# Kernel optimization log

Hardware: AMD Instinct MI355X
Metric: run time of the kernel (lower is better)

Reference implementation:

```python
import jax, jax.numpy as jnp
import numpy as np
from jax import lax

HIDDEN = 1024; HEADS = 16; HEAD = 64; LAYERS = 4; MLP = 4096
PATCH = 16; TUBE = 2; CROP = 224; FRAMES = 16
GRID = CROP // PATCH          # 14
DEPTH = FRAMES // TUBE        # 8
N_TOK = DEPTH * GRID * GRID   # 1568
EPS = 1e-6
D_ROT = 2 * ((HEAD // 3) // 2)  # 20 per rotary axis (d, h, w); 4 dims left unrotated


def setup_inputs() -> dict:
    key = jax.random.key(0)
    ks = jax.random.split(key, 12)
    w = lambda k, shape: jax.random.normal(k, shape, jnp.float32) * 0.02
    L, H, M = LAYERS, HIDDEN, MLP
    return {
        "pixel_values_videos": jax.random.normal(ks[0], (2, FRAMES, 3, CROP, CROP), jnp.float32),
        "patch_w": w(ks[1], (H, 3, TUBE, PATCH, PATCH)),  # Conv3d OIDHW
        "patch_b": jnp.zeros((H,), jnp.float32),
        "ln1_g": jnp.ones((L, H), jnp.float32), "ln1_b": jnp.zeros((L, H), jnp.float32),
        "qw": w(ks[2], (L, H, H)), "qb": jnp.zeros((L, H), jnp.float32),
        "kw": w(ks[3], (L, H, H)), "kb": jnp.zeros((L, H), jnp.float32),
        "vw": w(ks[4], (L, H, H)), "vb": jnp.zeros((L, H), jnp.float32),
        "pw": w(ks[5], (L, H, H)), "pb": jnp.zeros((L, H), jnp.float32),
        "ln2_g": jnp.ones((L, H), jnp.float32), "ln2_b": jnp.zeros((L, H), jnp.float32),
        "fc1w": w(ks[6], (L, M, H)), "fc1b": jnp.zeros((L, M), jnp.float32),
        "fc2w": w(ks[7], (L, H, M)), "fc2b": jnp.zeros((L, H), jnp.float32),
        "lnf_g": jnp.ones((H,), jnp.float32), "lnf_b": jnp.zeros((H,), jnp.float32),
    }


def _layer_norm(x, g, b):
    mu = jnp.mean(x, axis=-1, keepdims=True)
    var = jnp.mean(jnp.square(x - mu), axis=-1, keepdims=True)
    return (x - mu) * lax.rsqrt(var + EPS) * g + b


def _position_ids():
    ids = jnp.arange(N_TOK)
    tpf = GRID * GRID
    d_pos = ids // tpf
    rem = ids - d_pos * tpf
    h_pos = rem // GRID
    w_pos = rem - h_pos * GRID
    return d_pos, h_pos, w_pos


def _rotate(x, pos):
    # x: (B, H, N, D); matches VJEPA2 rotate_queries_or_keys:
    # tiled (not interleaved) sin/cos * interleaved rotate-half.
    D = x.shape[-1]
    omega = 1.0 / (10000.0 ** (jnp.arange(D // 2, dtype=x.dtype) / (D / 2.0)))
    freq = pos.astype(x.dtype)[:, None] * omega              # (N, D/2)
    sin = jnp.concatenate([jnp.sin(freq)] * 2, axis=-1)      # (N, D) tiled (torch .repeat)
    cos = jnp.concatenate([jnp.cos(freq)] * 2, axis=-1)
    y = x.reshape(x.shape[:-1] + (D // 2, 2))
    y = jnp.stack([-y[..., 1], y[..., 0]], axis=-1).reshape(x.shape)
    return x * cos + y * sin


def _apply_rope(x, pos_ids):
    d_pos, h_pos, w_pos = pos_ids
    s0, s1, s2 = 0, D_ROT, 2 * D_ROT
    parts = [_rotate(x[..., s0:s1], d_pos), _rotate(x[..., s1:s2], h_pos),
             _rotate(x[..., s2:3 * D_ROT], w_pos)]
    if 3 * D_ROT < HEAD:
        parts.append(x[..., 3 * D_ROT:])
    return jnp.concatenate(parts, axis=-1)


def _forward(pixel_values_videos, patch_w, patch_b, ln1_g, ln1_b, qw, qb, kw, kb,
             vw, vb, pw, pb, ln2_g, ln2_b, fc1w, fc1b, fc2w, fc2b, lnf_g, lnf_b):
    B = pixel_values_videos.shape[0]
    x = jnp.transpose(pixel_values_videos, (0, 2, 1, 3, 4))  # (B, C, T, H, W)
    h = lax.conv_general_dilated(x, patch_w, window_strides=(TUBE, PATCH, PATCH),
                                 padding="VALID",
                                 dimension_numbers=("NCDHW", "OIDHW", "NCDHW"))
    h = h + patch_b[None, :, None, None, None]
    h = h.reshape(B, HIDDEN, -1).transpose(0, 2, 1)          # (B, N, HIDDEN)

    pos_ids = _position_ids()
    scale = HEAD ** -0.5

    for i in range(LAYERS):
        # attention block
        xn = _layer_norm(h, ln1_g[i], ln1_b[i])
        def heads(w_, b_):
            return (xn @ w_.T + b_).reshape(B, N_TOK, HEADS, HEAD).transpose(0, 2, 1, 3)
        q = _apply_rope(heads(qw[i], qb[i]), pos_ids)
        k = _apply_rope(heads(kw[i], kb[i]), pos_ids)
        v = heads(vw[i], vb[i])
        aw = jnp.einsum("bhnd,bhmd->bhnm", q, k) * scale
        aw = jax.nn.softmax(aw.astype(jnp.float32), axis=-1).astype(q.dtype)
        o = jnp.einsum("bhnm,bhmd->bhnd", aw, v)
        o = o.transpose(0, 2, 1, 3).reshape(B, N_TOK, HIDDEN)
        h = h + (o @ pw[i].T + pb[i])
        # MLP block
        xn = _layer_norm(h, ln2_g[i], ln2_b[i])
        m = jax.nn.gelu(xn @ fc1w[i].T + fc1b[i], approximate=False)
        h = h + (m @ fc2w[i].T + fc2b[i])

    return _layer_norm(h, lnf_g, lnf_b)


def reference(pixel_values_videos, patch_w, patch_b, ln1_g, ln1_b, qw, qb, kw, kb,
              vw, vb, pw, pb, ln2_g, ln2_b, fc1w, fc1b, fc2w, fc2b, lnf_g, lnf_b):
    return _forward(pixel_values_videos, patch_w, patch_b, ln1_g, ln1_b, qw, qb, kw, kb,
                    vw, vb, pw, pb, ln2_g, ln2_b, fc1w, fc1b, fc2w, fc2b, lnf_g, lnf_b)
```

## Files before the change

### kernel.cpp

```cpp
#include <hip/hip_runtime.h>
#include <math.h>

#define NTOK   1568
#define BATCH  2
#define HID    1024
#define MLPD   4096
#define NLAYER 4
#define ROWS   (BATCH*NTOK)
#define CONVK  1536

typedef __bf16 bf16x8 __attribute__((ext_vector_type(8)));
typedef __bf16 bf16x2 __attribute__((ext_vector_type(2)));
typedef float  f32x4  __attribute__((ext_vector_type(4)));

__device__ __forceinline__ unsigned short f2b(float f) {
  unsigned int u = __float_as_uint(f);
  unsigned int r = u + 0x7FFFu + ((u >> 16) & 1u);
  return (unsigned short)(r >> 16);
}
__device__ __forceinline__ float b2f(unsigned short s) {
  return __uint_as_float((unsigned int)s << 16);
}
__device__ __forceinline__ unsigned cvt2(float a, float b) {
  bf16x2 t;
  t[0] = (__bf16)a;
  t[1] = (__bf16)b;
  return __builtin_bit_cast(unsigned, t);
}
__device__ __forceinline__ float e2(float x) { return __builtin_amdgcn_exp2f(x); }

__device__ __forceinline__ void async16(const unsigned short* g, unsigned short* l) {
  __builtin_amdgcn_global_load_lds(
      (__attribute__((address_space(1))) void*)(void*)g,
      (__attribute__((address_space(3))) void*)(void*)l, 16, 0, 0);
}

__global__ __launch_bounds__(256) void cast4_k(const float* __restrict__ s,
                                               unsigned short* __restrict__ d,
                                               long long n4) {
  long long i = (long long)blockIdx.x * 256 + threadIdx.x;
  long long stride = (long long)gridDim.x * 256;
  for (; i < n4; i += stride) {
    float4 v = ((const float4*)s)[i];
    *(ushort4*)(d + i * 4) = make_ushort4(f2b(v.x), f2b(v.y), f2b(v.z), f2b(v.w));
  }
}

__global__ __launch_bounds__(256) void castqkv_k(const float* __restrict__ q,
                                                 const float* __restrict__ k,
                                                 const float* __restrict__ v,
                                                 unsigned short* __restrict__ dst) {
  const float* src = blockIdx.y == 0 ? q : (blockIdx.y == 1 ? k : v);
  long long i4 = (long long)blockIdx.x * 256 + threadIdx.x;
  long long e = i4 * 4;
  int layer = (int)(e >> 20);
  long long de = e + ((long long)(2 * layer + blockIdx.y) << 20);
  float4 val = ((const float4*)src)[i4];
  *(ushort4*)(dst + de) = make_ushort4(f2b(val.x), f2b(val.y), f2b(val.z), f2b(val.w));
}

__global__ __launch_bounds__(256) void biascat_k(const float* __restrict__ qb,
                                                 const float* __restrict__ kb,
                                                 const float* __restrict__ vb,
                                                 float* __restrict__ dst) {
  int idx = blockIdx.x * 256 + threadIdx.x;
  int layer = idx / 3072, c = idx % 3072;
  float v = c < 1024 ? qb[layer * 1024 + c]
            : (c < 2048 ? kb[layer * 1024 + c - 1024] : vb[layer * 1024 + c - 2048]);
  dst[idx] = v;
}

__global__ __launch_bounds__(256) void im2col_k(const float* __restrict__ pv,
                                                unsigned short* __restrict__ A) {
  int idx = blockIdx.x * 256 + threadIdx.x;
  int row = idx / CONVK, col = idx % CONVK;
  int b = row / NTOK, t = row % NTOK;
  int d = t / 196, r = t % 196, hh = r / 14, ww = r % 14;
  int c = col >> 9, r2 = col & 511, td = r2 >> 8, ph = (r2 >> 4) & 15, pw = r2 & 15;
  int frame = 2 * d + td;
  const float* src = pv + ((((long long)b * 16 + frame) * 3 + c) * 224 + (hh * 16 + ph)) * 224
                        + (ww * 16 + pw);
  A[idx] = f2b(*src);
}

__global__ __launch_bounds__(512, 2) void gemm256(const unsigned short* __restrict__ A,
                                                  const unsigned short* __restrict__ B,
                                                  unsigned short* outP,
                                                  int M, int N, int K, int kChunk,
                                                  size_t zStride) {
  __shared__ unsigned short As[3][256 * 32];
  __shared__ unsigned short Bs[3][256 * 32];
  const int tid = threadIdx.x;
  const int lane = tid & 63;
  const int w = tid >> 6;
  const int wr = w >> 2, wc = w & 3;
  const int l15 = lane & 15, l4 = lane >> 4;
  const int wbase = tid & ~63;

  const int gx = gridDim.x, gy = gridDim.y;
  const int nwg = gx * gy * (int)gridDim.z;
  int orig = blockIdx.x + gx * (blockIdx.y + gy * blockIdx.z);
  int q = nwg >> 3, r = nwg & 7, xcd = orig & 7, idx = orig >> 3;
  int swz = (xcd < r ? xcd * (q + 1) : r * (q + 1) + (xcd - r) * q) + idx;
  const int bn = swz % gx;
  int tmp = swz / gx;
  const int bm = tmp % gy;
  const int bz = tmp / gy;
  const int kbeg = bz * kChunk;

  const int r0 = tid >> 2;
  const int g0 = (tid & 3) ^ ((tid >> 3) & 3);
  const int i1 = 512 + tid;
  const int r1 = i1 >> 2;
  const int g1 = (tid & 3) ^ ((i1 >> 3) & 3);
  int ra0 = bm * 256 + r0; if (ra0 >= M) ra0 = M - 1;
  int ra1 = bm * 256 + r1; if (ra1 >= M) ra1 = M - 1;
  const int rb0 = bn * 256 + r0;
  const int rb1 = bn * 256 + r1;
  const size_t Ao0 = (size_t)ra0 * K + g0 * 8;
  const size_t Ao1 = (size_t)ra1 * K + g1 * 8;
  const size_t Bo0 = (size_t)rb0 * K + g0 * 8;
  const size_t Bo1 = (size_t)rb1 * K + g1 * 8;

  auto stA = [&](int buf, int k0) {
    async16(A + Ao0 + k0, &As[buf][wbase * 8]);
    async16(A + Ao1 + k0, &As[buf][4096 + wbase * 8]);
  };
  auto stB = [&](int buf, int k0) {
    async16(B + Bo0 + k0, &Bs[buf][wbase * 8]);
    async16(B + Bo1 + k0, &Bs[buf][4096 + wbase * 8]);
  };

  f32x4 acc[8][4] = {};
  const int nk = kChunk >> 5;

  stA(0, kbeg); stB(0, kbeg);
  stA(1, kbeg + 32); stB(1, kbeg + 32);

  const int pchunk = (l4 ^ ((l15 >> 1) & 3)) * 8;
  const int abase = (wr * 128 + l15) * 32 + pchunk;
  const int bbase = (wc * 64 + l15) * 32 + pchunk;

  int cur = 0;
  for (int kt = 0; kt < nk; ++kt) {
    if (kt + 1 < nk) {
      asm volatile("s_waitcnt vmcnt(4)" ::: "memory");
    } else {
      asm volatile("s_waitcnt vmcnt(0)" ::: "memory");
    }
    __builtin_amdgcn_s_barrier();
    __builtin_amdgcn_sched_barrier(0);
    const int prebuf = cur >= 1 ? cur - 1 : 2;
    const bool doPre = (kt + 2 < nk);
    const int kpre = kbeg + (kt + 2) * 32;

    if (doPre) stA(prebuf, kpre);
    bf16x8 bfr[4], af[4];
#pragma unroll
    for (int n = 0; n < 4; ++n)
      bfr[n] = *(const bf16x8*)&Bs[cur][bbase + n * 512];
#pragma unroll
    for (int m = 0; m < 4; ++m)
      af[m] = *(const bf16x8*)&As[cur][abase + m * 512];
    __builtin_amdgcn_s_setprio(1);
#pragma unroll
    for (int m = 0; m < 4; ++m)
#pragma unroll
      for (int n = 0; n < 4; ++n)
        acc[m][n] = __builtin_amdgcn_mfma_f32_16x16x32_bf16(af[m], bfr[n], acc[m][n], 0, 0, 0);
    __builtin_amdgcn_s_setprio(0);
    __builtin_amdgcn_sched_barrier(0);

    if (doPre) stB(prebuf, kpre);
#pragma unroll
    for (int m = 0; m < 4; ++m)
      af[m] = *(const bf16x8*)&As[cur][abase + (m + 4) * 512];
    __builtin_amdgcn_s_setprio(1);
#pragma unroll
    for (int m = 0; m < 4; ++m)
#pragma unroll
      for (int n = 0; n < 4; ++n)
        acc[m + 4][n] = __builtin_amdgcn_mfma_f32_16x16x32_bf16(af[m], bfr[n], acc[m + 4][n], 0, 0, 0);
    __builtin_amdgcn_s_setprio(0);
    __builtin_amdgcn_sched_barrier(0);

    cur = cur == 2 ? 0 : cur + 1;
  }

  unsigned short* pout = outP + (size_t)bz * zStride;
#pragma unroll
  for (int m = 0; m < 8; ++m) {
    int rowb = bm * 256 + wr * 128 + m * 16 + l4 * 4;
#pragma unroll
    for (int rr2 = 0; rr2 < 4; ++rr2) {
      int rr = rowb + rr2;
      if (rr >= M) continue;
#pragma unroll
      for (int n = 0; n < 4; ++n) {
        int col = bn * 256 + wc * 64 + n * 16 + l15;
        pout[(size_t)rr * N + col] = f2b(acc[m][n][rr2]);
      }
    }
  }
}

template <int NP, int GELU>
__global__ __launch_bounds__(256) void reduceN_k(const unsigned short* p,
                                                 const float* __restrict__ bias,
                                                 unsigned short* outB,
                                                 int MN, int N, size_t pStride) {
  int i8 = blockIdx.x * 256 + threadIdx.x;
  int e = i8 * 8;
  float acc[8];
#pragma unroll
  for (int j = 0; j < 8; ++j) acc[j] = 0.0f;
#pragma unroll
  for (int pp = 0; pp < NP; ++pp) {
    const unsigned short* src = p + (size_t)pp * pStride + e;
    ushort4 a0 = *(const ushort4*)src;
    ushort4 a1 = *(const ushort4*)(src + 4);
    acc[0] += b2f(a0.x); acc[1] += b2f(a0.y); acc[2] += b2f(a0.z); acc[3] += b2f(a0.w);
    acc[4] += b2f(a1.x); acc[5] += b2f(a1.y); acc[6] += b2f(a1.z); acc[7] += b2f(a1.w);
  }
  int col = e % N;
  float4 b0 = *(const float4*)(bias + col);
  float4 b1 = *(const float4*)(bias + col + 4);
  acc[0] += b0.x; acc[1] += b0.y; acc[2] += b0.z; acc[3] += b0.w;
  acc[4] += b1.x; acc[5] += b1.y; acc[6] += b1.z; acc[7] += b1.w;
  if (GELU) {
#pragma unroll
    for (int j = 0; j < 8; ++j)
      acc[j] = 0.5f * acc[j] * (1.0f + erff(acc[j] * 0.70710678118654752f));
  }
  *(ushort4*)(outB + e) = make_ushort4(f2b(acc[0]), f2b(acc[1]), f2b(acc[2]), f2b(acc[3]));
  *(ushort4*)(outB + e + 4) = make_ushort4(f2b(acc[4]), f2b(acc[5]), f2b(acc[6]), f2b(acc[7]));
}

template <int NP, int RESID, int FINAL>
__global__ __launch_bounds__(256) void redln_k(const unsigned short* __restrict__ p,
                                               const float* __restrict__ bias,
                                               const float* resid,
                                               const float* __restrict__ g,
                                               const float* __restrict__ b,
                                               float* hOut,
                                               unsigned short* __restrict__ xnOut,
                                               float* __restrict__ fOut,
                                               size_t pStride) {
  __shared__ float red[8];
  const int row = blockIdx.x, tid = threadIdx.x;
  const int col = tid * 4;
  const size_t off = (size_t)row * HID + col;
  float v0 = 0, v1 = 0, v2 = 0, v3 = 0;
#pragma unroll
  for (int pp = 0; pp < NP; ++pp) {
    ushort4 a = *(const ushort4*)(p + (size_t)pp * pStride + off);
    v0 += b2f(a.x); v1 += b2f(a.y); v2 += b2f(a.z); v3 += b2f(a.w);
  }
  float4 bs = *(const float4*)(bias + col);
  v0 += bs.x; v1 += bs.y; v2 += bs.z; v3 += bs.w;
  if (RESID) {
    float4 r = *(const float4*)(resid + off);
    v0 += r.x; v1 += r.y; v2 += r.z; v3 += r.w;
  }
  if (!FINAL) *(float4*)(hOut + off) = make_float4(v0, v1, v2, v3);
  float s = v0 + v1 + v2 + v3;
  float q = v0 * v0 + v1 * v1 + v2 * v2 + v3 * v3;
  for (int o2 = 32; o2; o2 >>= 1) { s += __shfl_xor(s, o2); q += __shfl_xor(q, o2); }
  if ((tid & 63) == 0) { red[tid >> 6] = s; red[4 + (tid >> 6)] = q; }
  __syncthreads();
  float ts = red[0] + red[1] + red[2] + red[3];
  float tq = red[4] + red[5] + red[6] + red[7];
  float mu = ts * (1.0f / HID);
  float var = tq * (1.0f / HID) - mu * mu;
  float rs = rsqrtf(var + 1e-6f);
  float o0 = (v0 - mu) * rs * g[col + 0] + b[col + 0];
  float o1 = (v1 - mu) * rs * g[col + 1] + b[col + 1];
  float o2 = (v2 - mu) * rs * g[col + 2] + b[col + 2];
  float o3 = (v3 - mu) * rs * g[col + 3] + b[col + 3];
  if (FINAL) {
    *(float4*)(fOut + off) = make_float4(o0, o1, o2, o3);
  } else {
    *(ushort4*)(xnOut + off) = make_ushort4(f2b(o0), f2b(o1), f2b(o2), f2b(o3));
  }
}

__global__ __launch_bounds__(256) void qkvprep_k(const unsigned short* __restrict__ qkvb,
                                                 unsigned short* __restrict__ Qh,
                                                 unsigned short* __restrict__ Kh,
                                                 unsigned short* __restrict__ VT) {
  __shared__ unsigned short Vs[64 * 72];
  const int tile = blockIdx.x, bh = blockIdx.y;
  const int b = bh >> 4, head = bh & 15;
  const int tid = threadIdx.x;
  const int tl = tid >> 2, dc = tid & 3;
  const int tg = tile * 64 + tl;
  const int trc = tg < NTOK ? tg : NTOK - 1;
  const bool valid = tg < NTOK;
  const size_t srow = ((size_t)(b * NTOK + trc)) * 3072 + head * 64 + dc * 16;

  {
    uint4 v0 = *(const uint4*)(qkvb + srow + 2048);
    uint4 v1 = *(const uint4*)(qkvb + srow + 2048 + 8);
    *(uint4*)&Vs[tl * 72 + dc * 16] = v0;
    *(uint4*)&Vs[tl * 72 + dc * 16 + 8] = v1;
  }

  const int t = trc;
  const int dpos = t / 196, rem = t - dpos * 196, hpos = rem / 14, wpos = rem - hpos * 14;
  const float LG = 0.9210340371976184f;
  union V16 { uint4 u[2]; unsigned short s[16]; };
  V16 qin, kin, qout, kout;
  qin.u[0] = *(const uint4*)(qkvb + srow);
  qin.u[1] = *(const uint4*)(qkvb + srow + 8);
  kin.u[0] = *(const uint4*)(qkvb + srow + 1024);
  kin.u[1] = *(const uint4*)(qkvb + srow + 1024 + 8);
#pragma unroll
  for (int p = 0; p < 8; ++p) {
    int d0 = dc * 16 + 2 * p;
    float qx0 = b2f(qin.s[2 * p]), qx1 = b2f(qin.s[2 * p + 1]);
    float kx0 = b2f(kin.s[2 * p]), kx1 = b2f(kin.s[2 * p + 1]);
    float qo0, qo1, ko0, ko1;
    if (d0 >= 60) { qo0 = qx0; qo1 = qx1; ko0 = kx0; ko1 = kx1; }
    else {
      int region = d0 / 20;
      int j0 = d0 - region * 20;
      int pos = region == 0 ? dpos : (region == 1 ? hpos : wpos);
      float fp = (float)pos;
      int i0 = j0 % 10, i1 = (j0 + 1) % 10;
      float f0 = expf(-LG * (float)i0) * fp;
      float f1 = expf(-LG * (float)i1) * fp;
      float c0 = cosf(f0), s0 = sinf(f0), c1 = cosf(f1), s1 = sinf(f1);
      qo0 = qx0 * c0 - qx1 * s0; qo1 = qx1 * c1 + qx0 * s1;
      ko0 = kx0 * c0 - kx1 * s0; ko1 = kx1 * c1 + kx0 * s1;
    }
    const float QS = 0.18033688011112042f;
    qout.s[2 * p]     = f2b(qo0 * QS);
    qout.s[2 * p + 1] = f2b(qo1 * QS);
    kout.s[2 * p]     = f2b(ko0);
    kout.s[2 * p + 1] = f2b(ko1);
  }
  if (valid) {
    size_t drow = ((size_t)bh * NTOK + tg) * 64 + dc * 16;
    *(uint4*)(Qh + drow)     = qout.u[0];
    *(uint4*)(Qh + drow + 8) = qout.u[1];
    *(uint4*)(Kh + drow)     = kout.u[0];
    *(uint4*)(Kh + drow + 8) = kout.u[1];
  }
  __syncthreads();
  {
    int d = tid >> 2, tc = tid & 3;
    if (tile * 64 + tc * 16 < NTOK) {
      V16 o;
#pragma unroll
      for (int jj = 0; jj < 16; ++jj) o.s[jj] = Vs[(tc * 16 + jj) * 72 + d];
      unsigned short* dst = VT + ((size_t)bh * 64 + d) * NTOK + tile * 64 + tc * 16;
      *(uint4*)dst = o.u[0];
      *(uint4*)(dst + 8) = o.u[1];
    }
  }
}

__global__ __launch_bounds__(256, 4) void flash5_k(const unsigned short* __restrict__ Qh,
                                                   const unsigned short* __restrict__ Kh,
                                                   const unsigned short* __restrict__ VT,
                                                   unsigned short* __restrict__ Opart,
                                                   float2* __restrict__ ml) {
  __shared__ unsigned short Ks[2][64 * 64];
  __shared__ unsigned short Vs[2][64 * 64];
  const int bh = blockIdx.x, qt = blockIdx.y, kv = blockIdx.z;
  const int kt0 = kv ? 13 : 0, kt1 = kv ? 25 : 13;
  const int tid = threadIdx.x, lane = tid & 63, w = tid >> 6;
  const int l15 = lane & 15, l4 = lane >> 4;
  const size_t hb = (size_t)bh * NTOK * 64;
  const unsigned short* kgp = Kh + hb;
  const unsigned short* vbp = VT + (size_t)bh * 64 * NTOK;

  const int srow0 = w * 8 + (lane >> 3);
  const int scg0  = (lane & 7) ^ (srow0 & 7);
  const int srow1 = srow0 + 32;
  const int scg1  = (lane & 7) ^ (srow1 & 7);

  const int qrow = qt * 64 + w * 16 + l15;
  const int qrc = qrow < NTOK ? qrow : NTOK - 1;
  bf16x8 q0 = *(const bf16x8*)(Qh + hb + (size_t)qrc * 64 + l4 * 8);
  bf16x8 q1 = *(const bf16x8*)(Qh + hb + (size_t)qrc * 64 + 32 + l4 * 8);

  f32x4 oacc[4] = {};
  float m = -1e30f, l = 0.0f;

  {
    const int kc0 = kt0 * 64;
    async16(kgp + (size_t)(kc0 + srow0) * 64 + scg0 * 8, &Ks[0][(size_t)w * 512]);
    async16(kgp + (size_t)(kc0 + srow1) * 64 + scg1 * 8, &Ks[0][(size_t)(w + 4) * 512]);
    async16(vbp + (size_t)srow0 * NTOK + kc0 + scg0 * 8, &Vs[0][(size_t)w * 512]);
    async16(vbp + (size_t)srow1 * NTOK + kc0 + scg1 * 8, &Vs[0][(size_t)(w + 4) * 512]);
  }

  const int h7 = l15 & 7;
  const int p1 = (l4 ^ h7) * 8;
  const int p2 = ((l4 + 4) ^ h7) * 8;

  for (int kt = kt0; kt < kt1; ++kt) {
    const int cur = (kt - kt0) & 1, nxt = cur ^ 1;
    const int kb = kt * 64;
    __syncthreads();

    if (kt + 1 < kt1) {
      const int kn = kb + 64;
      async16(kgp + (size_t)(kn + srow0) * 64 + scg0 * 8, &Ks[nxt][(size_t)w * 512]);
      async16(kgp + (size_t)(kn + srow1) * 64 + scg1 * 8, &Ks[nxt][(size_t)(w + 4) * 512]);
      async16(vbp + (size_t)srow0 * NTOK + kn + scg0 * 8, &Vs[nxt][(size_t)w * 512]);
      async16(vbp + (size_t)srow1 * NTOK + kn + scg1 * 8, &Vs[nxt][(size_t)(w + 4) * 512]);
    }

    bf16x8 kc0[4], kc1[4];
#pragma unroll
    for (int nt = 0; nt < 4; ++nt) {
      const unsigned short* kr = &Ks[cur][(nt * 16 + l15) * 64];
      kc0[nt] = *(const bf16x8*)(kr + p1);
      kc1[nt] = *(const bf16x8*)(kr + p2);
    }
    f32x4 s[4] = {};
    __builtin_amdgcn_s_setprio(1);
#pragma unroll
    for (int nt = 0; nt < 4; ++nt) {
      s[nt] = __builtin_amdgcn_mfma_f32_16x16x32_bf16(kc0[nt], q0, s[nt], 0, 0, 0);
      s[nt] = __builtin_amdgcn_mfma_f32_16x16x32_bf16(kc1[nt], q1, s[nt], 0, 0, 0);
    }
    __builtin_amdgcn_s_setprio(0);
    bf16x8 vf0[4], vf1[4];
#pragma unroll
    for (int dt = 0; dt < 4; ++dt) {
      const unsigned short* vr = &Vs[cur][(dt * 16 + l15) * 64];
      vf0[dt] = *(const bf16x8*)(vr + p1);
      vf1[dt] = *(const bf16x8*)(vr + p2);
    }

    if (kb + 64 > NTOK) {
#pragma unroll
      for (int nt = 0; nt < 4; ++nt)
#pragma unroll
        for (int r = 0; r < 4; ++r)
          if (kb + nt * 16 + l4 * 4 + r >= NTOK) s[nt][r] = -1e30f;
    }
    float rmax = s[0][0];
#pragma unroll
    for (int nt = 0; nt < 4; ++nt)
#pragma unroll
      for (int r = 0; r < 4; ++r) rmax = fmaxf(rmax, s[nt][r]);
    rmax = fmaxf(rmax, __shfl_xor(rmax, 16));
    rmax = fmaxf(rmax, __shfl_xor(rmax, 32));
    if (!__all(rmax - m <= 11.5f)) {
      float mn = fmaxf(m, rmax);
      float alpha = e2(m - mn);
      m = mn;
      l *= alpha;
#pragma unroll
      for (int dt = 0; dt < 4; ++dt)
#pragma unroll
        for (int r = 0; r < 4; ++r) oacc[dt][r] *= alpha;
    }
    float rsum = 0.0f;
#pragma unroll
    for (int nt = 0; nt < 4; ++nt)
#pragma unroll
      for (int r = 0; r < 4; ++r) {
        float p = e2(s[nt][r] - m);
        s[nt][r] = p;
        rsum += p;
      }
    rsum += __shfl_xor(rsum, 16);
    rsum += __shfl_xor(rsum, 32);
    l += rsum;

    unsigned pk01[4], pk23[4];
#pragma unroll
    for (int nt = 0; nt < 4; ++nt) {
      pk01[nt] = cvt2(s[nt][0], s[nt][1]);
      pk23[nt] = cvt2(s[nt][2], s[nt][3]);
    }
    const int srcA = ((l4 & 1) << 5) | l15;
    const int srcB = srcA + 16;
    const bool hi = (l4 >> 1) != 0;
    union PB { unsigned u[4]; bf16x8 v; } pf[2];
#pragma unroll
    for (int kc = 0; kc < 2; ++kc) {
      unsigned t0, t1;
      t0 = __shfl(pk01[2 * kc], srcA); t1 = __shfl(pk01[2 * kc + 1], srcA);
      pf[kc].u[0] = hi ? t1 : t0;
      t0 = __shfl(pk23[2 * kc], srcA); t1 = __shfl(pk23[2 * kc + 1], srcA);
      pf[kc].u[1] = hi ? t1 : t0;
      t0 = __shfl(pk01[2 * kc], srcB); t1 = __shfl(pk01[2 * kc + 1], srcB);
      pf[kc].u[2] = hi ? t1 : t0;
      t0 = __shfl(pk23[2 * kc], srcB); t1 = __shfl(pk23[2 * kc + 1], srcB);
      pf[kc].u[3] = hi ? t1 : t0;
    }
    __builtin_amdgcn_s_setprio(1);
#pragma unroll
    for (int dt = 0; dt < 4; ++dt) {
      oacc[dt] = __builtin_amdgcn_mfma_f32_16x16x32_bf16(vf0[dt], pf[0].v, oacc[dt], 0, 0, 0);
      oacc[dt] = __builtin_amdgcn_mfma_f32_16x16x32_bf16(vf1[dt], pf[1].v, oacc[dt], 0, 0, 0);
    }
    __builtin_amdgcn_s_setprio(0);
  }

  __syncthreads();
  unsigned short* Os = &Ks[0][0];
#pragma unroll
  for (int dt = 0; dt < 4; ++dt)
#pragma unroll
    for (int r = 0; r < 4; ++r)
      Os[w * 1152 + l15 * 72 + dt * 16 + l4 * 4 + r] = f2b(oacc[dt][r]);
  if (qrow < NTOK) {
    uint4 a  = *(const uint4*)&Os[w * 1152 + l15 * 72 + l4 * 16];
    uint4 bq = *(const uint4*)&Os[w * 1152 + l15 * 72 + l4 * 16 + 8];
    unsigned short* op = Opart + ((size_t)(kv * 32 + bh) * NTOK + qrow) * 64;
    *(uint4*)(op + l4 * 16) = a;
    *(uint4*)(op + l4 * 16 + 8) = bq;
    if (l4 == 0) ml[(size_t)(kv * 32 + bh) * NTOK + qrow] = make_float2(m, l);
  }
}

__global__ __launch_bounds__(256) void fcomb_k(const unsigned short* __restrict__ Op,
                                               const float2* __restrict__ ml,
                                               unsigned short* __restrict__ O) {
  const int bh = blockIdx.x, qt = blockIdx.y;
  const int tid = threadIdx.x;
  const int qr = qt * 64 + (tid >> 2);
  const int dc = (tid & 3) * 16;
  if (qr >= NTOK) return;
  const int b = bh >> 4, head = bh & 15;
  float2 a0 = ml[(size_t)bh * NTOK + qr];
  float2 a1 = ml[(size_t)(32 + bh) * NTOK + qr];
  float M = fmaxf(a0.x, a1.x);
  float w0 = e2(a0.x - M), w1 = e2(a1.x - M);
  float inv = 1.0f / (a0.y * w0 + a1.y * w1);
  w0 *= inv; w1 *= inv;
  union V16 { uint4 u[2]; unsigned short s[16]; } p0, p1, o;
  const unsigned short* q0 = Op + ((size_t)bh * NTOK + qr) * 64 + dc;
  const unsigned short* q1 = Op + ((size_t)(32 + bh) * NTOK + qr) * 64 + dc;
  p0.u[0] = *(const uint4*)q0;       p0.u[1] = *(const uint4*)(q0 + 8);
  p1.u[0] = *(const uint4*)q1;       p1.u[1] = *(const uint4*)(q1 + 8);
#pragma unroll
  for (int j = 0; j < 16; ++j) o.s[j] = f2b(b2f(p0.s[j]) * w0 + b2f(p1.s[j]) * w1);
  unsigned short* dst = O + ((size_t)(b * NTOK + qr)) * HID + head * 64 + dc;
  *(uint4*)dst = o.u[0];
  *(uint4*)(dst + 8) = o.u[1];
}

extern "C" void kernel_launch(void* const* d_in, const int* in_sizes, int n_in,
                              void* d_out, int out_size, void* d_ws, size_t ws_size,
                              hipStream_t stream) {
  (void)in_sizes; (void)n_in; (void)out_size; (void)ws_size;
  const float* pv      = (const float*)d_in[0];
  const float* patch_w = (const float*)d_in[1];
  const float* patch_b = (const float*)d_in[2];
  const float* ln1_g   = (const float*)d_in[3];
  const float* ln1_b   = (const float*)d_in[4];
  const float* qw = (const float*)d_in[5];
  const float* qb = (const float*)d_in[6];
  const float* kw = (const float*)d_in[7];
  const float* kb = (const float*)d_in[8];
  const float* vw = (const float*)d_in[9];
  const float* vb = (const float*)d_in[10];
  const float* pw = (const float*)d_in[11];
  const float* pb = (const float*)d_in[12];
  const float* ln2_g = (const float*)d_in[13];
  const float* ln2_b = (const float*)d_in[14];
  const float* fc1w = (const float*)d_in[15];
  const float* fc1b = (const float*)d_in[16];
  const float* fc2w = (const float*)d_in[17];
  const float* fc2b = (const float*)d_in[18];
  const float* lnf_g = (const float*)d_in[19];
  const float* lnf_b = (const float*)d_in[20];

  char* wsp = (char*)d_ws;
  auto alloc = [&](size_t bytes) {
    char* p = wsp;
    wsp += (bytes + 255) & ~(size_t)255;
    return p;
  };
  unsigned short* wPatch = (unsigned short*)alloc((size_t)1024 * 1536 * 2);
  unsigned short* wQKV   = (unsigned short*)alloc((size_t)NLAYER * 3072 * 1024 * 2);
  unsigned short* wP     = (unsigned short*)alloc((size_t)NLAYER * HID * HID * 2);
  unsigned short* wF1    = (unsigned short*)alloc((size_t)NLAYER * MLPD * HID * 2);
  unsigned short* wF2    = (unsigned short*)alloc((size_t)NLAYER * HID * MLPD * 2);
  float*          qkvbias = (float*)alloc((size_t)NLAYER * 3072 * 4);
  unsigned short* Aim  = (unsigned short*)alloc((size_t)ROWS * CONVK * 2);
  float*          h    = (float*)alloc((size_t)ROWS * HID * 4);
  unsigned short* xnb  = (unsigned short*)alloc((size_t)ROWS * HID * 2);
  unsigned short* qkvo = (unsigned short*)alloc((size_t)ROWS * 3072 * 2);
  unsigned short* Qh   = (unsigned short*)alloc((size_t)ROWS * HID * 2 + 8192);
  unsigned short* Kh   = (unsigned short*)alloc((size_t)ROWS * HID * 2 + 8192);
  unsigned short* VT   = (unsigned short*)alloc((size_t)ROWS * HID * 2 + 8192);
  unsigned short* ob   = (unsigned short*)alloc((size_t)ROWS * HID * 2);
  unsigned short* mb   = (unsigned short*)alloc((size_t)ROWS * MLPD * 2);

  unsigned short* part  = Qh;
  unsigned short* partM = mb;
  unsigned short* Opart = mb;
  float2*         mlbuf = (float2*)(mb + (size_t)2 * 32 * NTOK * 64);
  const size_t MNs = (size_t)ROWS * HID;

  auto cast = [&](const float* s, unsigned short* d, long long n) {
    long long n4 = n / 4;
    int grid = (int)((n4 + 255) / 256);
    if (grid > 16384) grid = 16384;
    cast4_k<<<grid, 256, 0, stream>>>(s, d, n4);
  };
  cast(patch_w, wPatch, (long long)1024 * 1536);
  castqkv_k<<<dim3(4096, 3), 256, 0, stream>>>(qw, kw, vw, wQKV);
  cast(pw, wP, (long long)NLAYER * HID * HID);
  cast(fc1w, wF1, (long long)NLAYER * MLPD * HID);
  cast(fc2w, wF2, (long long)NLAYER * HID * MLPD);
  biascat_k<<<48, 256, 0, stream>>>(qb, kb, vb, qkvbias);

  im2col_k<<<(ROWS * CONVK) / 256, 256, 0, stream>>>(pv, Aim);
  gemm256<<<dim3(4, 13, 4), 512, 0, stream>>>(Aim, wPatch, part, ROWS, HID, CONVK, 384, MNs);
  redln_k<4, 0, 0><<<ROWS, 256, 0, stream>>>(
      part, patch_b, nullptr, ln1_g, ln1_b, h, xnb, nullptr, MNs);

  for (int i = 0; i < NLAYER; ++i) {
    gemm256<<<dim3(12, 13, 1), 512, 0, stream>>>(
        xnb, wQKV + (size_t)i * 3072 * 1024, part, ROWS, 3072, HID, 1024,
        (size_t)ROWS * 3072);
    reduceN_k<1, 0><<<(ROWS * 3072) / 2048, 256, 0, stream>>>(
        part, qkvbias + i * 3072, qkvo, ROWS * 3072, 3072, (size_t)ROWS * 3072);
    qkvprep_k<<<dim3(25, 32), 256, 0, stream>>>(qkvo, Qh, Kh, VT);
    flash5_k<<<dim3(32, 25, 2), 256, 0, stream>>>(Qh, Kh, VT, Opart, mlbuf);
    fcomb_k<<<dim3(32, 25), 256, 0, stream>>>(Opart, mlbuf, ob);
    gemm256<<<dim3(4, 13, 4), 512, 0, stream>>>(
        ob, wP + (size_t)i * HID * HID, partM, ROWS, HID, HID, 256, MNs);
    redln_k<4, 1, 0><<<ROWS, 256, 0, stream>>>(
        partM, pb + i * HID, h, ln2_g + i * HID, ln2_b + i * HID, h, xnb, nullptr, MNs);
    gemm256<<<dim3(16, 13, 1), 512, 0, stream>>>(
        xnb, wF1 + (size_t)i * MLPD * HID, part, ROWS, MLPD, HID, 1024, MNs);
    reduceN_k<1, 1><<<(ROWS * MLPD) / 2048, 256, 0, stream>>>(
        part, fc1b + i * MLPD, mb, ROWS * MLPD, MLPD, MNs);
    gemm256<<<dim3(4, 13, 4), 512, 0, stream>>>(
        mb, wF2 + (size_t)i * HID * MLPD, part, ROWS, HID, MLPD, 1024, MNs);
    if (i < NLAYER - 1) {
      redln_k<4, 1, 0><<<ROWS, 256, 0, stream>>>(
          part, fc2b + i * HID, h, ln1_g + (i + 1) * HID, ln1_b + (i + 1) * HID,
          h, xnb, nullptr, MNs);
    } else {
      redln_k<4, 1, 1><<<ROWS, 256, 0, stream>>>(
          part, fc2b + i * HID, h, lnf_g, lnf_b, nullptr, nullptr, (float*)d_out, MNs);
    }
  }
}
```

Measured before the change: 1.305 ms.

## Fuse bias/GELU into GEMM epilogue and process two query tiles per flash wave

Result: no change. 1.308 ms (+0.2%).

```diff
diff --git a/kernel.cpp b/kernel.cpp
--- a/kernel.cpp
+++ b/kernel.cpp
@@ -83,11 +83,13 @@
   A[idx] = f2b(*src);
 }
 
+template <int EPI>
 __global__ __launch_bounds__(512, 2) void gemm256(const unsigned short* __restrict__ A,
                                                   const unsigned short* __restrict__ B,
                                                   unsigned short* outP,
                                                   int M, int N, int K, int kChunk,
-                                                  size_t zStride) {
+                                                  size_t zStride,
+                                                  const float* __restrict__ bias) {
   __shared__ unsigned short As[3][256 * 32];
   __shared__ unsigned short Bs[3][256 * 32];
   const int tid = threadIdx.x;
@@ -187,6 +189,12 @@
     cur = cur == 2 ? 0 : cur + 1;
   }
 
+  float bsv[4] = {0, 0, 0, 0};
+  if (EPI >= 1) {
+#pragma unroll
+    for (int n = 0; n < 4; ++n)
+      bsv[n] = bias[bn * 256 + wc * 64 + n * 16 + l15];
+  }
   unsigned short* pout = outP + (size_t)bz * zStride;
 #pragma unroll
   for (int m = 0; m < 8; ++m) {
@@ -198,42 +206,13 @@
 #pragma unroll
       for (int n = 0; n < 4; ++n) {
         int col = bn * 256 + wc * 64 + n * 16 + l15;
-        pout[(size_t)rr * N + col] = f2b(acc[m][n][rr2]);
+        float v = acc[m][n][rr2];
+        if (EPI >= 1) v += bsv[n];
+        if (EPI == 2) v = 0.5f * v * (1.0f + erff(v * 0.70710678118654752f));
+        pout[(size_t)rr * N + col] = f2b(v);
       }
     }
   }
-}
-
-template <int NP, int GELU>
-__global__ __launch_bounds__(256) void reduceN_k(const unsigned short* p,
-                                                 const float* __restrict__ bias,
-                                                 unsigned short* outB,
-                                                 int MN, int N, size_t pStride) {
-  int i8 = blockIdx.x * 256 + threadIdx.x;
-  int e = i8 * 8;
-  float acc[8];
-#pragma unroll
-  for (int j = 0; j < 8; ++j) acc[j] = 0.0f;
-#pragma unroll
-  for (int pp = 0; pp < NP; ++pp) {
-    const unsigned short* src = p + (size_t)pp * pStride + e;
-    ushort4 a0 = *(const ushort4*)src;
-    ushort4 a1 = *(const ushort4*)(src + 4);
-    acc[0] += b2f(a0.x); acc[1] += b2f(a0.y); acc[2] += b2f(a0.z); acc[3] += b2f(a0.w);
-    acc[4] += b2f(a1.x); acc[5] += b2f(a1.y); acc[6] += b2f(a1.z); acc[7] += b2f(a1.w);
-  }
-  int col = e % N;
-  float4 b0 = *(const float4*)(bias + col);
-  float4 b1 = *(const float4*)(bias + col + 4);
-  acc[0] += b0.x; acc[1] += b0.y; acc[2] += b0.z; acc[3] += b0.w;
-  acc[4] += b1.x; acc[5] += b1.y; acc[6] += b1.z; acc[7] += b1.w;
-  if (GELU) {
-#pragma unroll
-    for (int j = 0; j < 8; ++j)
-      acc[j] = 0.5f * acc[j] * (1.0f + erff(acc[j] * 0.70710678118654752f));
-  }
-  *(ushort4*)(outB + e) = make_ushort4(f2b(acc[0]), f2b(acc[1]), f2b(acc[2]), f2b(acc[3]));
-  *(ushort4*)(outB + e + 4) = make_ushort4(f2b(acc[4]), f2b(acc[5]), f2b(acc[6]), f2b(acc[7]));
 }
 
 template <int NP, int RESID, int FINAL>
@@ -360,7 +339,51 @@
   }
 }
 
-__global__ __launch_bounds__(256, 4) void flash5_k(const unsigned short* __restrict__ Qh,
+#define SM_BLOCK(S, MREG, LREG, OACC, PF)                                        \
+  {                                                                              \
+    float rmax = S[0][0];                                                        \
+    _Pragma("unroll") for (int nt = 0; nt < 4; ++nt)                             \
+      _Pragma("unroll") for (int rr = 0; rr < 4; ++rr)                           \
+        rmax = fmaxf(rmax, S[nt][rr]);                                           \
+    rmax = fmaxf(rmax, __shfl_xor(rmax, 16));                                    \
+    rmax = fmaxf(rmax, __shfl_xor(rmax, 32));                                    \
+    if (!__all(rmax - MREG <= 11.5f)) {                                          \
+      float mn = fmaxf(MREG, rmax);                                              \
+      float alpha = e2(MREG - mn);                                               \
+      MREG = mn;                                                                 \
+      LREG *= alpha;                                                             \
+      _Pragma("unroll") for (int dt = 0; dt < 4; ++dt)                           \
+        _Pragma("unroll") for (int rr = 0; rr < 4; ++rr) OACC[dt][rr] *= alpha;  \
+    }                                                                            \
+    float rsum = 0.0f;                                                           \
+    _Pragma("unroll") for (int nt = 0; nt < 4; ++nt)                             \
+      _Pragma("unroll") for (int rr = 0; rr < 4; ++rr) {                         \
+        float pv = e2(S[nt][rr] - MREG);                                         \
+        S[nt][rr] = pv;                                                          \
+        rsum += pv;                                                              \
+      }                                                                          \
+    rsum += __shfl_xor(rsum, 16);                                                \
+    rsum += __shfl_xor(rsum, 32);                                                \
+    LREG += rsum;                                                                \
+    unsigned pk01[4], pk23[4];                                                   \
+    _Pragma("unroll") for (int nt = 0; nt < 4; ++nt) {                           \
+      pk01[nt] = cvt2(S[nt][0], S[nt][1]);                                       \
+      pk23[nt] = cvt2(S[nt][2], S[nt][3]);                                       \
+    }                                                                            \
+    _Pragma("unroll") for (int kc = 0; kc < 2; ++kc) {                           \
+      unsigned t0, t1;                                                           \
+      t0 = __shfl(pk01[2 * kc], srcA); t1 = __shfl(pk01[2 * kc + 1], srcA);      \
+      PF[kc].u[0] = hi ? t1 : t0;                                                \
+      t0 = __shfl(pk23[2 * kc], srcA); t1 = __shfl(pk23[2 * kc + 1], srcA);      \
+      PF[kc].u[1] = hi ? t1 : t0;                                                \
+      t0 = __shfl(pk01[2 * kc], srcB); t1 = __shfl(pk01[2 * kc + 1], srcB);      \
+      PF[kc].u[2] = hi ? t1 : t0;                                                \
+      t0 = __shfl(pk23[2 * kc], srcB); t1 = __shfl(pk23[2 * kc + 1], srcB);      \
+      PF[kc].u[3] = hi ? t1 : t0;                                                \
+    }                                                                            \
+  }
+
+__global__ __launch_bounds__(256, 3) void flash6_k(const unsigned short* __restrict__ Qh,
                                                    const unsigned short* __restrict__ Kh,
                                                    const unsigned short* __restrict__ VT,
                                                    unsigned short* __restrict__ Opart,
@@ -380,13 +403,17 @@
   const int srow1 = srow0 + 32;
   const int scg1  = (lane & 7) ^ (srow1 & 7);
 
-  const int qrow = qt * 64 + w * 16 + l15;
-  const int qrc = qrow < NTOK ? qrow : NTOK - 1;
-  bf16x8 q0 = *(const bf16x8*)(Qh + hb + (size_t)qrc * 64 + l4 * 8);
-  bf16x8 q1 = *(const bf16x8*)(Qh + hb + (size_t)qrc * 64 + 32 + l4 * 8);
-
-  f32x4 oacc[4] = {};
-  float m = -1e30f, l = 0.0f;
+  const int qrow0 = qt * 128 + w * 32 + l15;
+  const int qrow1 = qrow0 + 16;
+  const int qrc0 = qrow0 < NTOK ? qrow0 : NTOK - 1;
+  const int qrc1 = qrow1 < NTOK ? qrow1 : NTOK - 1;
+  bf16x8 qa0 = *(const bf16x8*)(Qh + hb + (size_t)qrc0 * 64 + l4 * 8);
+  bf16x8 qa1 = *(const bf16x8*)(Qh + hb + (size_t)qrc0 * 64 + 32 + l4 * 8);
+  bf16x8 qb0 = *(const bf16x8*)(Qh + hb + (size_t)qrc1 * 64 + l4 * 8);
+  bf16x8 qb1 = *(const bf16x8*)(Qh + hb + (size_t)qrc1 * 64 + 32 + l4 * 8);
+
+  f32x4 oaccA[4] = {}, oaccB[4] = {};
+  float mA = -1e30f, lA = 0.0f, mB = -1e30f, lB = 0.0f;
 
   {
     const int kc0 = kt0 * 64;
@@ -399,6 +426,9 @@
   const int h7 = l15 & 7;
   const int p1 = (l4 ^ h7) * 8;
   const int p2 = ((l4 + 4) ^ h7) * 8;
+  const int srcA = ((l4 & 1) << 5) | l15;
+  const int srcB = srcA + 16;
+  const bool hi = (l4 >> 1) != 0;
 
   for (int kt = kt0; kt < kt1; ++kt) {
     const int cur = (kt - kt0) & 1, nxt = cur ^ 1;
@@ -420,12 +450,14 @@
       kc0[nt] = *(const bf16x8*)(kr + p1);
       kc1[nt] = *(const bf16x8*)(kr + p2);
     }
-    f32x4 s[4] = {};
+    f32x4 sA[4] = {}, sB[4] = {};
     __builtin_amdgcn_s_setprio(1);
 #pragma unroll
     for (int nt = 0; nt < 4; ++nt) {
-      s[nt] = __builtin_amdgcn_mfma_f32_16x16x32_bf16(kc0[nt], q0, s[nt], 0, 0, 0);
-      s[nt] = __builtin_amdgcn_mfma_f32_16x16x32_bf16(kc1[nt], q1, s[nt], 0, 0, 0);
+      sA[nt] = __builtin_amdgcn_mfma_f32_16x16x32_bf16(kc0[nt], qa0, sA[nt], 0, 0, 0);
+      sA[nt] = __builtin_amdgcn_mfma_f32_16x16x32_bf16(kc1[nt], qa1, sA[nt], 0, 0, 0);
+      sB[nt] = __builtin_amdgcn_mfma_f32_16x16x32_bf16(kc0[nt], qb0, sB[nt], 0, 0, 0);
+      sB[nt] = __builtin_amdgcn_mfma_f32_16x16x32_bf16(kc1[nt], qb1, sB[nt], 0, 0, 0);
     }
     __builtin_amdgcn_s_setprio(0);
     bf16x8 vf0[4], vf1[4];
@@ -440,66 +472,25 @@
 #pragma unroll
       for (int nt = 0; nt < 4; ++nt)
 #pragma unroll
-        for (int r = 0; r < 4; ++r)
-          if (kb + nt * 16 + l4 * 4 + r >= NTOK) s[nt][r] = -1e30f;
-    }
-    float rmax = s[0][0];
-#pragma unroll
-    for (int nt = 0; nt < 4; ++nt)
-#pragma unroll
-      for (int r = 0; r < 4; ++r) rmax = fmaxf(rmax, s[nt][r]);
-    rmax = fmaxf(rmax, __shfl_xor(rmax, 16));
-    rmax = fmaxf(rmax, __shfl_xor(rmax, 32));
-    if (!__all(rmax - m <= 11.5f)) {
-      float mn = fmaxf(m, rmax);
-      float alpha = e2(m - mn);
-      m = mn;
-      l *= alpha;
-#pragma unroll
-      for (int dt = 0; dt < 4; ++dt)
-#pragma unroll
-        for (int r = 0; r < 4; ++r) oacc[dt][r] *= alpha;
-    }
-    float rsum = 0.0f;
-#pragma unroll
-    for (int nt = 0; nt < 4; ++nt)
-#pragma unroll
-      for (int r = 0; r < 4; ++r) {
-        float p = e2(s[nt][r] - m);
-        s[nt][r] = p;
-        rsum += p;
-      }
-    rsum += __shfl_xor(rsum, 16);
-    rsum += __shfl_xor(rsum, 32);
-    l += rsum;
-
-    unsigned pk01[4], pk23[4];
-#pragma unroll
-    for (int nt = 0; nt < 4; ++nt) {
-      pk01[nt] = cvt2(s[nt][0], s[nt][1]);
-      pk23[nt] = cvt2(s[nt][2], s[nt][3]);
-    }
-    const int srcA = ((l4 & 1) << 5) | l15;
-    const int srcB = srcA + 16;
-    const bool hi = (l4 >> 1) != 0;
-    union PB { unsigned u[4]; bf16x8 v; } pf[2];
-#pragma unroll
-    for (int kc = 0; kc < 2; ++kc) {
-      unsigned t0, t1;
-      t0 = __shfl(pk01[2 * kc], srcA); t1 = __shfl(pk01[2 * kc + 1], srcA);
-      pf[kc].u[0] = hi ? t1 : t0;
-      t0 = __shfl(pk23[2 * kc], srcA); t1 = __shfl(pk23[2 * kc + 1], srcA);
-      pf[kc].u[1] = hi ? t1 : t0;
-      t0 = __shfl(pk01[2 * kc], srcB); t1 = __shfl(pk01[2 * kc + 1], srcB);
-      pf[kc].u[2] = hi ? t1 : t0;
-      t0 = __shfl(pk23[2 * kc], srcB); t1 = __shfl(pk23[2 * kc + 1], srcB);
-      pf[kc].u[3] = hi ? t1 : t0;
-    }
+        for (int rr = 0; rr < 4; ++rr)
+          if (kb + nt * 16 + l4 * 4 + rr >= NTOK) { sA[nt][rr] = -1e30f; sB[nt][rr] = -1e30f; }
+    }
+
+    union PB { unsigned u[4]; bf16x8 v; } pfA[2], pfB[2];
+    SM_BLOCK(sA, mA, lA, oaccA, pfA)
     __builtin_amdgcn_s_setprio(1);
 #pragma unroll
     for (int dt = 0; dt < 4; ++dt) {
-      oacc[dt] = __builtin_amdgcn_mfma_f32_16x16x32_bf16(vf0[dt], pf[0].v, oacc[dt], 0, 0, 0);
-      oacc[dt] = __builtin_amdgcn_mfma_f32_16x16x32_bf16(vf1[dt], pf[1].v, oacc[dt], 0, 0, 0);
+      oaccA[dt] = __builtin_amdgcn_mfma_f32_16x16x32_bf16(vf0[dt], pfA[0].v, oaccA[dt], 0, 0, 0);
+      oaccA[dt] = __builtin_amdgcn_mfma_f32_16x16x32_bf16(vf1[dt], pfA[1].v, oaccA[dt], 0, 0, 0);
+    }
+    __builtin_amdgcn_s_setprio(0);
+    SM_BLOCK(sB, mB, lB, oaccB, pfB)
+    __builtin_amdgcn_s_setprio(1);
+#pragma unroll
+    for (int dt = 0; dt < 4; ++dt) {
+      oaccB[dt] = __builtin_amdgcn_mfma_f32_16x16x32_bf16(vf0[dt], pfB[0].v, oaccB[dt], 0, 0, 0);
+      oaccB[dt] = __builtin_amdgcn_mfma_f32_16x16x32_bf16(vf1[dt], pfB[1].v, oaccB[dt], 0, 0, 0);
     }
     __builtin_amdgcn_s_setprio(0);
   }
@@ -509,15 +500,29 @@
 #pragma unroll
   for (int dt = 0; dt < 4; ++dt)
 #pragma unroll
-    for (int r = 0; r < 4; ++r)
-      Os[w * 1152 + l15 * 72 + dt * 16 + l4 * 4 + r] = f2b(oacc[dt][r]);
-  if (qrow < NTOK) {
+    for (int rr = 0; rr < 4; ++rr)
+      Os[w * 1152 + l15 * 72 + dt * 16 + l4 * 4 + rr] = f2b(oaccA[dt][rr]);
+  if (qrow0 < NTOK) {
     uint4 a  = *(const uint4*)&Os[w * 1152 + l15 * 72 + l4 * 16];
     uint4 bq = *(const uint4*)&Os[w * 1152 + l15 * 72 + l4 * 16 + 8];
-    unsigned short* op = Opart + ((size_t)(kv * 32 + bh) * NTOK + qrow) * 64;
+    unsigned short* op = Opart + ((size_t)(kv * 32 + bh) * NTOK + qrow0) * 64;
     *(uint4*)(op + l4 * 16) = a;
     *(uint4*)(op + l4 * 16 + 8) = bq;
-    if (l4 == 0) ml[(size_t)(kv * 32 + bh) * NTOK + qrow] = make_float2(m, l);
+    if (l4 == 0) ml[(size_t)(kv * 32 + bh) * NTOK + qrow0] = make_float2(mA, lA);
+  }
+  __builtin_amdgcn_sched_barrier(0);
+#pragma unroll
+  for (int dt = 0; dt < 4; ++dt)
+#pragma unroll
+    for (int rr = 0; rr < 4; ++rr)
+      Os[w * 1152 + l15 * 72 + dt * 16 + l4 * 4 + rr] = f2b(oaccB[dt][rr]);
+  if (qrow1 < NTOK) {
+    uint4 a  = *(const uint4*)&Os[w * 1152 + l15 * 72 + l4 * 16];
+    uint4 bq = *(const uint4*)&Os[w * 1152 + l15 * 72 + l4 * 16 + 8];
+    unsigned short* op = Opart + ((size_t)(kv * 32 + bh) * NTOK + qrow1) * 64;
+    *(uint4*)(op + l4 * 16) = a;
+    *(uint4*)(op + l4 * 16 + 8) = bq;
+    if (l4 == 0) ml[(size_t)(kv * 32 + bh) * NTOK + qrow1] = make_float2(mB, lB);
   }
 }
 
@@ -616,29 +621,27 @@
   biascat_k<<<48, 256, 0, stream>>>(qb, kb, vb, qkvbias);
 
   im2col_k<<<(ROWS * CONVK) / 256, 256, 0, stream>>>(pv, Aim);
-  gemm256<<<dim3(4, 13, 4), 512, 0, stream>>>(Aim, wPatch, part, ROWS, HID, CONVK, 384, MNs);
+  gemm256<0><<<dim3(4, 13, 4), 512, 0, stream>>>(
+      Aim, wPatch, part, ROWS, HID, CONVK, 384, MNs, nullptr);
   redln_k<4, 0, 0><<<ROWS, 256, 0, stream>>>(
       part, patch_b, nullptr, ln1_g, ln1_b, h, xnb, nullptr, MNs);
 
   for (int i = 0; i < NLAYER; ++i) {
-    gemm256<<<dim3(12, 13, 1), 512, 0, stream>>>(
-        xnb, wQKV + (size_t)i * 3072 * 1024, part, ROWS, 3072, HID, 1024,
-        (size_t)ROWS * 3072);
-    reduceN_k<1, 0><<<(ROWS * 3072) / 2048, 256, 0, stream>>>(
-        part, qkvbias + i * 3072, qkvo, ROWS * 3072, 3072, (size_t)ROWS * 3072);
+    gemm256<1><<<dim3(12, 13, 1), 512, 0, stream>>>(
+        xnb, wQKV + (size_t)i * 3072 * 1024, qkvo, ROWS, 3072, HID, 1024,
+        0, qkvbias + i * 3072);
     qkvprep_k<<<dim3(25, 32), 256, 0, stream>>>(qkvo, Qh, Kh, VT);
-    flash5_k<<<dim3(32, 25, 2), 256, 0, stream>>>(Qh, Kh, VT, Opart, mlbuf);
+    flash6_k<<<dim3(32, 13, 2), 256, 0, stream>>>(Qh, Kh, VT, Opart, mlbuf);
     fcomb_k<<<dim3(32, 25), 256, 0, stream>>>(Opart, mlbuf, ob);
-    gemm256<<<dim3(4, 13, 4), 512, 0, stream>>>(
-        ob, wP + (size_t)i * HID * HID, partM, ROWS, HID, HID, 256, MNs);
+    gemm256<0><<<dim3(4, 13, 4), 512, 0, stream>>>(
+        ob, wP + (size_t)i * HID * HID, partM, ROWS, HID, HID, 256, MNs, nullptr);
     redln_k<4, 1, 0><<<ROWS, 256, 0, stream>>>(
         partM, pb + i * HID, h, ln2_g + i * HID, ln2_b + i * HID, h, xnb, nullptr, MNs);
-    gemm256<<<dim3(16, 13, 1), 512, 0, stream>>>(
-        xnb, wF1 + (size_t)i * MLPD * HID, part, ROWS, MLPD, HID, 1024, MNs);
-    reduceN_k<1, 1><<<(ROWS * MLPD) / 2048, 256, 0, stream>>>(
-        part, fc1b + i * MLPD, mb, ROWS * MLPD, MLPD, MNs);
-    gemm256<<<dim3(4, 13, 4), 512, 0, stream>>>(
-        mb, wF2 + (size_t)i * HID * MLPD, part, ROWS, HID, MLPD, 1024, MNs);
+    gemm256<2><<<dim3(16, 13, 1), 512, 0, stream>>>(
+        xnb, wF1 + (size_t)i * MLPD * HID, mb, ROWS, MLPD, HID, 1024,
+        0, fc1b + i * MLPD);
+    gemm256<0><<<dim3(4, 13, 4), 512, 0, stream>>>(
+        mb, wF2 + (size_t)i * HID * MLPD, part, ROWS, HID, MLPD, 1024, MNs, nullptr);
     if (i < NLAYER - 1) {
       redln_k<4, 1, 0><<<ROWS, 256, 0, stream>>>(
           part, fc2b + i * HID, h, ln1_g + (i + 1) * HID, ln1_b + (i + 1) * HID,
```
